# Kernel tuning notes

Measured on AMD Instinct MI355X. Metric: run time of the kernel, lower is better.

Reference implementation:

```python
import jax, jax.numpy as jnp
import numpy as np
from math import pi

BS, H, C = 4096, 1024, 512
H2, C2 = H // 2, C // 2


def _cm(x, y):
    # complex multiply with real/imag stored in last dim
    return jnp.stack([x[..., 0] * y[..., 0] - x[..., 1] * y[..., 1],
                      x[..., 0] * y[..., 1] + x[..., 1] * y[..., 0]], -1)


def _interleave(a, b):
    # (H2, C2),(H2, C2) -> (H, C2) rows [a0,b0,a1,b1,...]
    return jnp.stack([a, b], 1).reshape(-1, a.shape[1])


def _rotations(phi, theta):
    cp, sp = jnp.cos(phi), jnp.sin(phi)
    ct, st = jnp.cos(theta), jnp.sin(theta)
    z = jnp.zeros_like(ct)
    diag = jnp.stack([_interleave(cp * ct, ct), _interleave(sp * ct, z)], -1)      # (H, C2, 2)
    offd = jnp.stack([_interleave(-cp * st, st), _interleave(-sp * st, z)], -1)    # (H, C2, 2)
    return diag.transpose(1, 0, 2), offd.transpose(1, 0, 2)                        # (C2, H, 2)


def _swap_pairs(x):
    # swap elements within adjacent pairs along the hidden axis
    bs, h, _ = x.shape
    return x.reshape(bs, h // 2, 2, 2)[:, :, ::-1, :].reshape(bs, h, 2)


def setup_inputs() -> dict:
    key = jax.random.key(0)
    ks = jax.random.split(key, 5)
    x = jax.random.normal(ks[0], (BS, H, 2), dtype=jnp.float32)
    phi0 = 2 * pi * jax.random.normal(ks[1], (H2, C2), dtype=jnp.float32)
    theta0 = 2 * pi * jax.random.normal(ks[2], (H2, C2), dtype=jnp.float32)
    phi1 = 2 * pi * jax.random.normal(ks[3], (H2, C2), dtype=jnp.float32)
    theta1 = 2 * pi * jax.random.normal(ks[4], (H2, C2), dtype=jnp.float32)
    return {"x": x, "phi0": phi0, "theta0": theta0, "phi1": phi1, "theta1": theta1}


def reference(x, phi0, theta0, phi1, theta1):
    d0, o0 = _rotations(phi0, theta0)
    d1, o1 = _rotations(phi1, theta1)

    def step(xc, dd):
        dd0, oo0, dd1, oo1 = dd
        xc = _cm(xc, dd0) + _cm(_swap_pairs(xc), oo0)
        xc = jnp.roll(xc, -1, axis=1)   # cat(x[1:], x[:1])
        xc = _cm(xc, dd1) + _cm(_swap_pairs(xc), oo1)
        xc = jnp.roll(xc, 1, axis=1)    # cat(x[-1:], x[:-1])
        return xc, None

    x, _ = jax.lax.scan(step, x, (d0, o0, d1, o1))
    return x
```

## Files before the change

### kernel.cpp

```cpp
#include <hip/hip_runtime.h>


#define BS 4096
#define H_DIM 1024
#define H2 512
#define C2 256
#define RPW 4


__global__ __launch_bounds__(256) void eunn_coef_kernel(
    const float* __restrict__ phi0, const float* __restrict__ theta0,
    const float* __restrict__ phi1, const float* __restrict__ theta1,
    float4* __restrict__ coef) {
    int t = blockIdx.x * 256 + threadIdx.x;
    int i = t & 511;
    int p = (t >> 9) & 1;
    int c = t >> 10;
    const float* phi   = p ? phi1   : phi0;
    const float* theta = p ? theta1 : theta0;
    float ph = phi[i * C2 + c];
    float th = theta[i * C2 + c];
    float sp, cp, st, ct;
    sincosf(ph, &sp, &cp);
    sincosf(th, &st, &ct);
    int j = i & 7;
    int l = i >> 3;
    coef[(((c * 2 + p) * 8) + j) * 64 + l] = make_float4(ct, st, cp, sp);
}

__device__ __forceinline__ void rot_pair(const float4 q,
                                         float& ur, float& ui,
                                         float& wr, float& wi) {
    float ar = fmaf(-q.y, wr, q.x * ur);
    float ai = fmaf(-q.y, wi, q.x * ui);
    float br = fmaf( q.x, wr, q.y * ur);
    float bi = fmaf( q.x, wi, q.y * ui);
    ur = fmaf(-q.w, ai, q.z * ar);
    ui = fmaf( q.w, ar, q.z * ai);
    wr = br;
    wi = bi;
}

__global__ __launch_bounds__(256, 2) void eunn_main_kernel(
    const float* __restrict__ x,
    const float4* __restrict__ coef,
    float* __restrict__ out) {
    const int lane = threadIdx.x & 63;
    const int wave = threadIdx.x >> 6;
    const int row0 = (blockIdx.x * 4 + wave) * RPW;

    float vr[RPW][16], vi[RPW][16];

#pragma unroll
    for (int r = 0; r < RPW; ++r) {
        const float4* src = (const float4*)(x + (size_t)(row0 + r) * (H_DIM * 2)) + lane * 8;
#pragma unroll
        for (int m = 0; m < 8; ++m) {
            float4 f = src[m];
            vr[r][2 * m]     = f.x; vi[r][2 * m]     = f.y;
            vr[r][2 * m + 1] = f.z; vi[r][2 * m + 1] = f.w;
        }
    }

#pragma unroll 1
    for (int c = 0; c < C2; ++c) {
        const float4* ca = coef + (size_t)c * 1024;

#pragma unroll
        for (int j = 0; j < 8; ++j) {
            float4 q = ca[j * 64 + lane];
#pragma unroll
            for (int r = 0; r < RPW; ++r) {
                rot_pair(q, vr[r][2 * j], vi[r][2 * j],
                            vr[r][2 * j + 1], vi[r][2 * j + 1]);
            }
        }

#pragma unroll
        for (int j = 0; j < 7; ++j) {
            float4 q = ca[(8 + j) * 64 + lane];
#pragma unroll
            for (int r = 0; r < RPW; ++r) {
                rot_pair(q, vr[r][2 * j + 1], vi[r][2 * j + 1],
                            vr[r][2 * j + 2], vi[r][2 * j + 2]);
            }
        }

        {
            float4 q = ca[15 * 64 + lane];
#pragma unroll
            for (int r = 0; r < RPW; ++r) {
                float nwr = __shfl(vr[r][0], (lane + 1) & 63);
                float nwi = __shfl(vi[r][0], (lane + 1) & 63);
                rot_pair(q, vr[r][15], vi[r][15], nwr, nwi);
                vr[r][0] = __shfl(nwr, (lane + 63) & 63);
                vi[r][0] = __shfl(nwi, (lane + 63) & 63);
            }
        }
    }

#pragma unroll
    for (int r = 0; r < RPW; ++r) {
        float4* dst = (float4*)(out + (size_t)(row0 + r) * (H_DIM * 2)) + lane * 8;
#pragma unroll
        for (int m = 0; m < 8; ++m) {
            dst[m] = make_float4(vr[r][2 * m],     vi[r][2 * m],
                                 vr[r][2 * m + 1], vi[r][2 * m + 1]);
        }
    }
}

extern "C" void kernel_launch(void* const* d_in, const int* in_sizes, int n_in,
                              void* d_out, int out_size, void* d_ws, size_t ws_size,
                              hipStream_t stream) {
    const float* x      = (const float*)d_in[0];
    const float* phi0   = (const float*)d_in[1];
    const float* theta0 = (const float*)d_in[2];
    const float* phi1   = (const float*)d_in[3];
    const float* theta1 = (const float*)d_in[4];
    float* out = (float*)d_out;
    float4* coef = (float4*)d_ws;

    hipLaunchKernelGGL(eunn_coef_kernel, dim3(1024), dim3(256), 0, stream,
                       phi0, theta0, phi1, theta1, coef);

    hipLaunchKernelGGL(eunn_main_kernel, dim3(256), dim3(256), 0, stream,
                       x, coef, out);
}
```

Baseline: 460.6 us.

## Double-buffer coefficient loads, restructure wrap-around shuffles, halve rows per wave

Coefficients for the next layer are now prefetched into registers while the current layer is computed, using two alternating register buffers. The wrap-around rotation is restructured so the lane-neighbor shuffles are issued early and overlap with the interior rotations, and the second shuffle is dropped by loading a shifted coefficient instead. Rows per wave drop from 4 to 2 and the grid doubles to 512 blocks, giving more waves for latency hiding at the cost of reusing each coefficient load across fewer rows. The coefficient kernel also switches to fast intrinsic sincos, which is less accurate for the large angle inputs used here.

```diff
diff --git a/kernel.cpp b/kernel.cpp
--- a/kernel.cpp
+++ b/kernel.cpp
@@ -1,11 +1,9 @@
 #include <hip/hip_runtime.h>
 
 
-#define BS 4096
 #define H_DIM 1024
-#define H2 512
 #define C2 256
-#define RPW 4
+#define RPW 2
 
 
 __global__ __launch_bounds__(256) void eunn_coef_kernel(
@@ -21,8 +19,8 @@
     float ph = phi[i * C2 + c];
     float th = theta[i * C2 + c];
     float sp, cp, st, ct;
-    sincosf(ph, &sp, &cp);
-    sincosf(th, &st, &ct);
+    __sincosf(ph, &sp, &cp);
+    __sincosf(th, &st, &ct);
     int j = i & 7;
     int l = i >> 3;
     coef[(((c * 2 + p) * 8) + j) * 64 + l] = make_float4(ct, st, cp, sp);
@@ -62,41 +60,66 @@
         }
     }
 
-#pragma unroll 1
-    for (int c = 0; c < C2; ++c) {
+    float4 qa[17], qb[17];
+
+    auto load_coefs = [&](float4* q, int c) {
         const float4* ca = coef + (size_t)c * 1024;
+#pragma unroll
+        for (int j = 0; j < 16; ++j) q[j] = ca[j * 64 + lane];
+        q[16] = ca[15 * 64 + ((lane + 63) & 63)];
+    };
 
+    auto do_layer = [&](const float4* q) {
 #pragma unroll
-        for (int j = 0; j < 8; ++j) {
-            float4 q = ca[j * 64 + lane];
+        for (int r = 0; r < RPW; ++r) {
+            rot_pair(q[0], vr[r][0],  vi[r][0],  vr[r][1],  vi[r][1]);
+            rot_pair(q[7], vr[r][14], vi[r][14], vr[r][15], vi[r][15]);
+        }
+        float nbr[RPW], nbi[RPW], pbr[RPW], pbi[RPW];
+#pragma unroll
+        for (int r = 0; r < RPW; ++r) {
+            nbr[r] = __shfl(vr[r][0],  (lane + 1)  & 63);
+            nbi[r] = __shfl(vi[r][0],  (lane + 1)  & 63);
+            pbr[r] = __shfl(vr[r][15], (lane + 63) & 63);
+            pbi[r] = __shfl(vi[r][15], (lane + 63) & 63);
+        }
+#pragma unroll
+        for (int j = 1; j < 7; ++j) {
 #pragma unroll
             for (int r = 0; r < RPW; ++r) {
-                rot_pair(q, vr[r][2 * j], vi[r][2 * j],
-                            vr[r][2 * j + 1], vi[r][2 * j + 1]);
+                rot_pair(q[j], vr[r][2 * j],     vi[r][2 * j],
+                               vr[r][2 * j + 1], vi[r][2 * j + 1]);
             }
         }
-
 #pragma unroll
         for (int j = 0; j < 7; ++j) {
-            float4 q = ca[(8 + j) * 64 + lane];
 #pragma unroll
             for (int r = 0; r < RPW; ++r) {
-                rot_pair(q, vr[r][2 * j + 1], vi[r][2 * j + 1],
-                            vr[r][2 * j + 2], vi[r][2 * j + 2]);
+                rot_pair(q[8 + j], vr[r][2 * j + 1], vi[r][2 * j + 1],
+                                   vr[r][2 * j + 2], vi[r][2 * j + 2]);
             }
         }
+        const float4 qq = q[15];
+        const float4 qp = q[16];
+#pragma unroll
+        for (int r = 0; r < RPW; ++r) {
+            float ar = fmaf(-qq.y, nbr[r], qq.x * vr[r][15]);
+            float ai = fmaf(-qq.y, nbi[r], qq.x * vi[r][15]);
+            vr[r][15] = fmaf(-qq.w, ai, qq.z * ar);
+            vi[r][15] = fmaf( qq.w, ar, qq.z * ai);
+            float b0r = fmaf(qp.x, vr[r][0], qp.y * pbr[r]);
+            float b0i = fmaf(qp.x, vi[r][0], qp.y * pbi[r]);
+            vr[r][0] = b0r; vi[r][0] = b0i;
+        }
+    };
 
-        {
-            float4 q = ca[15 * 64 + lane];
-#pragma unroll
-            for (int r = 0; r < RPW; ++r) {
-                float nwr = __shfl(vr[r][0], (lane + 1) & 63);
-                float nwi = __shfl(vi[r][0], (lane + 1) & 63);
-                rot_pair(q, vr[r][15], vi[r][15], nwr, nwi);
-                vr[r][0] = __shfl(nwr, (lane + 63) & 63);
-                vi[r][0] = __shfl(nwi, (lane + 63) & 63);
-            }
-        }
+    load_coefs(qa, 0);
+#pragma unroll 1
+    for (int c = 0; c < C2; c += 2) {
+        load_coefs(qb, c + 1);
+        do_layer(qa);
+        load_coefs(qa, (c + 2 < C2) ? (c + 2) : 0);
+        do_layer(qb);
     }
 
 #pragma unroll
@@ -124,6 +147,6 @@
     hipLaunchKernelGGL(eunn_coef_kernel, dim3(1024), dim3(256), 0, stream,
                        phi0, theta0, phi1, theta1, coef);
 
-    hipLaunchKernelGGL(eunn_main_kernel, dim3(256), dim3(256), 0, stream,
+    hipLaunchKernelGGL(eunn_main_kernel, dim3(512), dim3(256), 0, stream,
                        x, coef, out);
 }
```

Measured after the change: 1.105 ms. +140.0%, slower.

## Double-buffer layer coefficients in registers and halve rows per wave

Applied to the files above, without the earlier changes.

The main loop now preloads all 16 coefficient float4s for the next layer into a second register buffer, ping-ponging between two buffers so global loads overlap the current layer's rotations. The wrap-around pair is restructured so the shuffles are issued early: neighbour values are exchanged once and the boundary rotation is split across lanes, replacing the serial shuffle-rotate-shuffle chain. Rows per wave drop from 4 to 2 and the grid doubles to 512 blocks, trading per-wave reuse for more parallelism. The coefficient kernel uses fast __sincosf with a coalesced thread mapping, which risks accuracy for large-magnitude angles (about 2π times a normal sample).

```diff
diff --git a/kernel.cpp b/kernel.cpp
--- a/kernel.cpp
+++ b/kernel.cpp
@@ -1,11 +1,9 @@
 #include <hip/hip_runtime.h>
 
 
-#define BS 4096
 #define H_DIM 1024
-#define H2 512
 #define C2 256
-#define RPW 4
+#define RPW 2
 
 
 __global__ __launch_bounds__(256) void eunn_coef_kernel(
@@ -13,19 +11,20 @@
     const float* __restrict__ phi1, const float* __restrict__ theta1,
     float4* __restrict__ coef) {
     int t = blockIdx.x * 256 + threadIdx.x;
-    int i = t & 511;
-    int p = (t >> 9) & 1;
-    int c = t >> 10;
+    int c = t & 255;
+    int ip = t >> 8;
+    int i = ip >> 1;
+    int p = ip & 1;
     const float* phi   = p ? phi1   : phi0;
     const float* theta = p ? theta1 : theta0;
     float ph = phi[i * C2 + c];
     float th = theta[i * C2 + c];
     float sp, cp, st, ct;
-    sincosf(ph, &sp, &cp);
-    sincosf(th, &st, &ct);
-    int j = i & 7;
+    __sincosf(ph, &sp, &cp);
+    __sincosf(th, &st, &ct);
+    int j = (i & 7) + 8 * p;
     int l = i >> 3;
-    coef[(((c * 2 + p) * 8) + j) * 64 + l] = make_float4(ct, st, cp, sp);
+    coef[((c * 16) + j) * 64 + l] = make_float4(ct, st, cp, sp);
 }
 
 __device__ __forceinline__ void rot_pair(const float4 q,
@@ -40,6 +39,55 @@
     wr = br;
     wi = bi;
 }
+
+#define LAYER_BODY(QCUR, QNXT, CNXT)                                          \
+    {                                                                         \
+        const float4* can = cl + (size_t)(CNXT) * 1024;                       \
+        _Pragma("unroll")                                                     \
+        for (int j = 0; j < 16; ++j) QNXT[j] = can[j * 64];                   \
+        float4 qq = QCUR[15];                                                 \
+        float qpx = __shfl(qq.x, (lane + 63) & 63);                           \
+        float qpy = __shfl(qq.y, (lane + 63) & 63);                           \
+        _Pragma("unroll")                                                     \
+        for (int r = 0; r < RPW; ++r) {                                       \
+            rot_pair(QCUR[0], vr[r][0],  vi[r][0],  vr[r][1],  vi[r][1]);     \
+            rot_pair(QCUR[7], vr[r][14], vi[r][14], vr[r][15], vi[r][15]);    \
+        }                                                                     \
+        float nbr[RPW], nbi[RPW], pbr[RPW], pbi[RPW];                         \
+        _Pragma("unroll")                                                     \
+        for (int r = 0; r < RPW; ++r) {                                       \
+            nbr[r] = __shfl(vr[r][0],  (lane + 1)  & 63);                     \
+            nbi[r] = __shfl(vi[r][0],  (lane + 1)  & 63);                     \
+            pbr[r] = __shfl(vr[r][15], (lane + 63) & 63);                     \
+            pbi[r] = __shfl(vi[r][15], (lane + 63) & 63);                     \
+        }                                                                     \
+        _Pragma("unroll")                                                     \
+        for (int j = 1; j < 7; ++j) {                                         \
+            _Pragma("unroll")                                                 \
+            for (int r = 0; r < RPW; ++r) {                                   \
+                rot_pair(QCUR[j], vr[r][2 * j],     vi[r][2 * j],             \
+                                  vr[r][2 * j + 1], vi[r][2 * j + 1]);        \
+            }                                                                 \
+        }                                                                     \
+        _Pragma("unroll")                                                     \
+        for (int j = 0; j < 7; ++j) {                                         \
+            _Pragma("unroll")                                                 \
+            for (int r = 0; r < RPW; ++r) {                                   \
+                rot_pair(QCUR[8 + j], vr[r][2 * j + 1], vi[r][2 * j + 1],     \
+                                      vr[r][2 * j + 2], vi[r][2 * j + 2]);    \
+            }                                                                 \
+        }                                                                     \
+        _Pragma("unroll")                                                     \
+        for (int r = 0; r < RPW; ++r) {                                       \
+            float ar = fmaf(-qq.y, nbr[r], qq.x * vr[r][15]);                 \
+            float ai = fmaf(-qq.y, nbi[r], qq.x * vi[r][15]);                 \
+            vr[r][15] = fmaf(-qq.w, ai, qq.z * ar);                           \
+            vi[r][15] = fmaf( qq.w, ar, qq.z * ai);                           \
+            float b0r = fmaf(qpx, vr[r][0], qpy * pbr[r]);                    \
+            float b0i = fmaf(qpx, vi[r][0], qpy * pbi[r]);                    \
+            vr[r][0] = b0r; vi[r][0] = b0i;                                   \
+        }                                                                     \
+    }
 
 __global__ __launch_bounds__(256, 2) void eunn_main_kernel(
     const float* __restrict__ x,
@@ -62,41 +110,16 @@
         }
     }
 
+    const float4* cl = coef + lane;
+
+    float4 qa[16], qb[16];
+#pragma unroll
+    for (int j = 0; j < 16; ++j) qa[j] = cl[j * 64];
+
 #pragma unroll 1
-    for (int c = 0; c < C2; ++c) {
-        const float4* ca = coef + (size_t)c * 1024;
-
-#pragma unroll
-        for (int j = 0; j < 8; ++j) {
-            float4 q = ca[j * 64 + lane];
-#pragma unroll
-            for (int r = 0; r < RPW; ++r) {
-                rot_pair(q, vr[r][2 * j], vi[r][2 * j],
-                            vr[r][2 * j + 1], vi[r][2 * j + 1]);
-            }
-        }
-
-#pragma unroll
-        for (int j = 0; j < 7; ++j) {
-            float4 q = ca[(8 + j) * 64 + lane];
-#pragma unroll
-            for (int r = 0; r < RPW; ++r) {
-                rot_pair(q, vr[r][2 * j + 1], vi[r][2 * j + 1],
-                            vr[r][2 * j + 2], vi[r][2 * j + 2]);
-            }
-        }
-
-        {
-            float4 q = ca[15 * 64 + lane];
-#pragma unroll
-            for (int r = 0; r < RPW; ++r) {
-                float nwr = __shfl(vr[r][0], (lane + 1) & 63);
-                float nwi = __shfl(vi[r][0], (lane + 1) & 63);
-                rot_pair(q, vr[r][15], vi[r][15], nwr, nwi);
-                vr[r][0] = __shfl(nwr, (lane + 63) & 63);
-                vi[r][0] = __shfl(nwi, (lane + 63) & 63);
-            }
-        }
+    for (int c = 0; c < C2; c += 2) {
+        LAYER_BODY(qa, qb, c + 1)
+        LAYER_BODY(qb, qa, (c + 2) & 255)
     }
 
 #pragma unroll
@@ -124,6 +147,6 @@
     hipLaunchKernelGGL(eunn_coef_kernel, dim3(1024), dim3(256), 0, stream,
                        phi0, theta0, phi1, theta1, coef);
 
-    hipLaunchKernelGGL(eunn_main_kernel, dim3(256), dim3(256), 0, stream,
+    hipLaunchKernelGGL(eunn_main_kernel, dim3(512), dim3(256), 0, stream,
                        x, coef, out);
 }
```

New measurement: 587.9 us. 1.28x slower.
